# Performance work log

Measured on AMD Instinct MI355X. Metric: run time of the kernel, lower is better.

## Reference

```python
import jax, jax.numpy as jnp
import numpy as np

B, S, D = 512, 64, 2048


def setup_inputs() -> dict:
    key = jax.random.key(0)
    ks = jax.random.split(key, 5)
    return {
        "classical_state": jax.random.normal(ks[0], (B, D), jnp.float32),
        "amplitudes": jax.random.normal(ks[1], (S, D), jnp.float32),
        "phases": jax.random.normal(ks[2], (S, D), jnp.float32),
        "rotation_gates": jax.random.normal(ks[3], (S, 2, 2), jnp.float32),
        "entanglement_matrix": jax.random.normal(ks[4], (S, S), jnp.float32),
    }


def reference(classical_state, amplitudes, phases, rotation_gates, entanglement_matrix):
    # classical_state: [B, D]; amplitudes/phases: [S, D]; rotation_gates: [S, 2, 2]
    b, d = classical_state.shape
    s = amplitudes.shape[0]

    # create_superposition
    norm_amp = amplitudes / jnp.linalg.norm(amplitudes, axis=1, keepdims=True)  # F.normalize p=2 dim=1
    real_amp = norm_amp * (jnp.cos(phases) + jnp.sin(phases))                   # [S, D]

    # _apply_quantum_rotation: per-pair (x[:, 2p:2p+2] @ gate) for each gate i -> vectorized over S and pairs
    xr = classical_state.reshape(b, d // 2, 2)                                  # [B, P, 2]
    rotated = jnp.einsum('bpi,sij->bspj', xr, rotation_gates).reshape(b, s, d)  # [B, S, D]

    states = real_amp[None, :, :] * rotated                                     # weighted superposition [B, S, D]

    # _apply_entanglement: softmax over rows then matmul across superposition dim
    ent_w = jax.nn.softmax(entanglement_matrix, axis=1)                          # [S, S]
    entangled = jnp.einsum('st,btd->bsd', ent_w, states)                         # [B, S, D]

    # collapse_superposition: multinomial over softmax(sum of squares), gather selected state
    logits = jnp.sum(entangled * entangled, axis=2)                              # [B, S]
    probabilities = jax.nn.softmax(logits, axis=1)
    outcome = jax.random.categorical(jax.random.key(42), logits, axis=1)         # [B] ~ multinomial(probabilities)
    collapsed = jnp.take_along_axis(entangled, outcome[:, None, None], axis=1)[:, 0, :]  # [B, D]
    return collapsed
```

## Files before the change

kernel.cpp:

```cpp
#include <hip/hip_runtime.h>
#include <math.h>

#define NB 512
#define NS 64
#define ND 2048
#define NP 1024

__device__ __forceinline__ unsigned rotl32(unsigned x, int d) {
    return (x << d) | (x >> (32 - d));
}

__device__ __forceinline__ void threefry2x32(unsigned k0, unsigned k1,
                                             unsigned& x0, unsigned& x1) {
    const unsigned ks0 = k0, ks1 = k1, ks2 = k0 ^ k1 ^ 0x1BD11BDAu;
    const int r0[4] = {13, 15, 26, 6};
    const int r1[4] = {17, 29, 16, 24};
    x0 += ks0; x1 += ks1;
#pragma unroll
    for (int i = 0; i < 4; ++i) { x0 += x1; x1 = rotl32(x1, r0[i]); x1 ^= x0; }
    x0 += ks1; x1 += ks2 + 1u;
#pragma unroll
    for (int i = 0; i < 4; ++i) { x0 += x1; x1 = rotl32(x1, r1[i]); x1 ^= x0; }
    x0 += ks2; x1 += ks0 + 2u;
#pragma unroll
    for (int i = 0; i < 4; ++i) { x0 += x1; x1 = rotl32(x1, r0[i]); x1 ^= x0; }
    x0 += ks0; x1 += ks1 + 3u;
#pragma unroll
    for (int i = 0; i < 4; ++i) { x0 += x1; x1 = rotl32(x1, r1[i]); x1 ^= x0; }
    x0 += ks1; x1 += ks2 + 4u;
#pragma unroll
    for (int i = 0; i < 4; ++i) { x0 += x1; x1 = rotl32(x1, r0[i]); x1 ^= x0; }
    x0 += ks2; x1 += ks0 + 5u;
}

__global__ void __launch_bounds__(1024)
k_MQ(const float* __restrict__ amp, const float* __restrict__ ph,
     const float* __restrict__ G, const float* __restrict__ E,
     float* __restrict__ M0, float* __restrict__ M1, float* __restrict__ Qt) {
    __shared__ float norm2[NS];
    __shared__ float W_l[NS], in_l[NS];
    __shared__ float Gl[NS * 4];
    __shared__ float4 part4[4][256];
    const int blk = blockIdx.x;
    const int tid = threadIdx.x;
    const int srow = blk >> 2;

    {
        const int r = tid >> 4, sub = tid & 15;
        const float4* a4 = (const float4*)(amp + r * ND);
        float acc = 0.f;
#pragma unroll 8
        for (int i = 0; i < 32; ++i) {
            float4 v = a4[sub + 16 * i];
            acc += v.x * v.x + v.y * v.y + v.z * v.z + v.w * v.w;
        }
        acc += __shfl_down(acc, 8, 16);
        acc += __shfl_down(acc, 4, 16);
        acc += __shfl_down(acc, 2, 16);
        acc += __shfl_down(acc, 1, 16);
        if (sub == 0) norm2[r] = acc;
    }
    if (tid < NS * 4) Gl[tid] = G[tid];
    __syncthreads();
    if (tid < NS) {
        in_l[tid] = 1.0f / sqrtf(norm2[tid]);
        float e = E[srow * NS + tid];
        float m = e;
        for (int off = 32; off; off >>= 1) m = fmaxf(m, __shfl_down(m, off));
        m = __shfl(m, 0);
        float ex = expf(e - m);
        float sum = ex;
        for (int off = 32; off; off >>= 1) sum += __shfl_down(sum, off);
        sum = __shfl(sum, 0);
        W_l[tid] = ex / sum;
    }
    __syncthreads();

    {
        const int pi = tid & 255;
        const int tg = tid >> 8;
        const int p = ((blk & 3) << 8) + pi;
        const int t0 = tg << 4;
        const float2* a2 = (const float2*)amp;
        const float2* p2 = (const float2*)ph;
        float a0 = 0.f, a1 = 0.f, b0 = 0.f, b1 = 0.f;
#pragma unroll 4
        for (int t = t0; t < t0 + 16; ++t) {
            float2 av = a2[t * NP + p];
            float2 pv = p2[t * NP + p];
            float w = W_l[t], in = in_l[t];
            float ra0 = av.x * in * (__cosf(pv.x) + __sinf(pv.x));
            float ra1 = av.y * in * (__cosf(pv.y) + __sinf(pv.y));
            float wr0 = w * ra0, wr1 = w * ra1;
            a0 += wr0 * Gl[4 * t + 0];
            b0 += wr0 * Gl[4 * t + 2];
            a1 += wr1 * Gl[4 * t + 1];
            b1 += wr1 * Gl[4 * t + 3];
        }
        part4[tg][pi] = make_float4(a0, a1, b0, b1);
    }
    __syncthreads();

    if (tid < 256) {
        const int p = ((blk & 3) << 8) + tid;
        float4 s0 = part4[0][tid], s1 = part4[1][tid],
               s2 = part4[2][tid], s3 = part4[3][tid];
        float a0 = s0.x + s1.x + s2.x + s3.x;
        float a1 = s0.y + s1.y + s2.y + s3.y;
        float b0 = s0.z + s1.z + s2.z + s3.z;
        float b1 = s0.w + s1.w + s2.w + s3.w;
        float2 m0v = {a0, a1}, m1v = {b0, b1};
        ((float2*)(M0 + srow * ND))[p] = m0v;
        ((float2*)(M1 + srow * ND))[p] = m1v;
        Qt[(3 * p + 0) * NS + srow] = a0 * a0 + a1 * a1;
        Qt[(3 * p + 1) * NS + srow] = a0 * b0 + a1 * b1;
        Qt[(3 * p + 2) * NS + srow] = b0 * b0 + b1 * b1;
    }
}

__global__ void __launch_bounds__(1024)
k_row(const float* __restrict__ x, const float* __restrict__ Qt,
      const float* __restrict__ M0, const float* __restrict__ M1,
      float* __restrict__ out) {
    __shared__ float2 xs[2 * NP];
    __shared__ float part[16][2][NS];
    __shared__ int o_sh[2];
    const int blk = blockIdx.x;
    const int tid = threadIdx.x;
    const int r0 = 2 * blk;

    ((float4*)xs)[tid] = ((const float4*)(x + r0 * ND))[tid];
    __syncthreads();

    const int w = tid >> 6, s = tid & 63;
    {
        float acc0 = 0.f, acc1 = 0.f;
        const int p0 = w << 6;
#pragma unroll 4
        for (int p = p0; p < p0 + 64; ++p) {
            float q0 = Qt[(3 * p + 0) * NS + s];
            float q1 = Qt[(3 * p + 1) * NS + s];
            float q2 = Qt[(3 * p + 2) * NS + s];
            float2 v0 = xs[p], v1 = xs[NP + p];
            acc0 += v0.x * v0.x * q0 + 2.f * v0.x * v0.y * q1 + v0.y * v0.y * q2;
            acc1 += v1.x * v1.x * q0 + 2.f * v1.x * v1.y * q1 + v1.y * v1.y * q2;
        }
        part[w][0][s] = acc0;
        part[w][1][s] = acc1;
    }
    __syncthreads();

    if (tid < 128) {
        const int w2 = tid >> 6;
        float l = 0.f;
#pragma unroll
        for (int k = 0; k < 16; ++k) l += part[k][w2][s];
        unsigned n = (unsigned)((r0 + w2) * NS + s);
        unsigned t0 = 0u, t1 = n;
        threefry2x32(0u, 42u, t0, t1);
        unsigned bits = t0 ^ t1;
        float u = (float)(bits >> 9) * (1.0f / 8388608.0f);
        u = fmaxf(u, 1.17549435e-38f);
        float g = -logf(-logf(u));
        float best = l + g;
        int bi = s;
        for (int off = 32; off; off >>= 1) {
            float ov = __shfl_down(best, off);
            int oi = __shfl_down(bi, off);
            if (ov > best || (ov == best && oi < bi)) { best = ov; bi = oi; }
        }
        if (s == 0) o_sh[w2] = bi;
    }
    __syncthreads();

#pragma unroll
    for (int r = 0; r < 2; ++r) {
        const int o = o_sh[r];
        const float2* m0p = (const float2*)(M0 + o * ND);
        const float2* m1p = (const float2*)(M1 + o * ND);
        const float2* xr = xs + r * NP;
        float2* op = (float2*)(out + (r0 + r) * ND);
        float2 xv = xr[tid], m0 = m0p[tid], m1 = m1p[tid];
        float2 rr;
        rr.x = xv.x * m0.x + xv.y * m1.x;
        rr.y = xv.x * m0.y + xv.y * m1.y;
        op[tid] = rr;
    }
}

extern "C" void kernel_launch(void* const* d_in, const int* in_sizes, int n_in,
                              void* d_out, int out_size, void* d_ws, size_t ws_size,
                              hipStream_t stream) {
    const float* x   = (const float*)d_in[0];
    const float* amp = (const float*)d_in[1];
    const float* ph  = (const float*)d_in[2];
    const float* G   = (const float*)d_in[3];
    const float* E   = (const float*)d_in[4];
    float* out = (float*)d_out;
    float* ws = (float*)d_ws;

    float* M0 = ws;
    float* M1 = ws + 131072;
    float* Qt = ws + 262144;

    k_MQ <<<256, 1024, 0, stream>>>(amp, ph, G, E, M0, M1, Qt);
    k_row<<<256, 1024, 0, stream>>>(x, Qt, M0, M1, out);
}
```

Measured before the change: 90.58 us.

## Fuse the two kernels into one with a software grid barrier

Merges the precompute kernel (M0/M1/Qt) and the per-row sampling kernel into one persistent launch of 256 blocks. A global atomic counter acts as a grid-wide barrier between the phases, and a second counter resets the barrier state at the end. Shared memory is reused between phases. This removes the second launch and the gap between kernels. It relies on all 256 blocks being resident at once and on the workspace counters starting in a consistent state; otherwise the spin-wait could deadlock.

```diff
diff --git a/kernel.cpp b/kernel.cpp
--- a/kernel.cpp
+++ b/kernel.cpp
@@ -5,6 +5,7 @@
 #define NS 64
 #define ND 2048
 #define NP 1024
+#define NBLK 256
 
 __device__ __forceinline__ unsigned rotl32(unsigned x, int d) {
     return (x << d) | (x >> (32 - d));
@@ -34,15 +35,20 @@
 }
 
 __global__ void __launch_bounds__(1024)
-k_MQ(const float* __restrict__ amp, const float* __restrict__ ph,
-     const float* __restrict__ G, const float* __restrict__ E,
-     float* __restrict__ M0, float* __restrict__ M1, float* __restrict__ Qt) {
+k_fused(const float* __restrict__ x, const float* __restrict__ amp,
+        const float* __restrict__ ph, const float* __restrict__ G,
+        const float* __restrict__ E, float* __restrict__ out,
+        int* __restrict__ bar, float* __restrict__ M0, float* __restrict__ M1,
+        float* __restrict__ Qt) {
+    __shared__ __align__(16) char smem[16384];
     __shared__ float norm2[NS];
     __shared__ float W_l[NS], in_l[NS];
     __shared__ float Gl[NS * 4];
-    __shared__ float4 part4[4][256];
+    __shared__ float partB[16][2][NS];
+    __shared__ int o_sh[2];
     const int blk = blockIdx.x;
     const int tid = threadIdx.x;
+    const int S = *(volatile int*)&bar[0];
     const int srow = blk >> 2;
 
     {
@@ -75,8 +81,8 @@
         W_l[tid] = ex / sum;
     }
     __syncthreads();
-
     {
+        float4* part4 = (float4*)smem;
         const int pi = tid & 255;
         const int tg = tid >> 8;
         const int p = ((blk & 3) << 8) + pi;
@@ -97,14 +103,14 @@
             a1 += wr1 * Gl[4 * t + 1];
             b1 += wr1 * Gl[4 * t + 3];
         }
-        part4[tg][pi] = make_float4(a0, a1, b0, b1);
-    }
-    __syncthreads();
-
+        part4[tg * 256 + pi] = make_float4(a0, a1, b0, b1);
+    }
+    __syncthreads();
     if (tid < 256) {
+        const float4* part4 = (const float4*)smem;
         const int p = ((blk & 3) << 8) + tid;
-        float4 s0 = part4[0][tid], s1 = part4[1][tid],
-               s2 = part4[2][tid], s3 = part4[3][tid];
+        float4 s0 = part4[0 * 256 + tid], s1 = part4[1 * 256 + tid],
+               s2 = part4[2 * 256 + tid], s3 = part4[3 * 256 + tid];
         float a0 = s0.x + s1.x + s2.x + s3.x;
         float a1 = s0.y + s1.y + s2.y + s3.y;
         float b0 = s0.z + s1.z + s2.z + s3.z;
@@ -116,75 +122,87 @@
         Qt[(3 * p + 1) * NS + srow] = a0 * b0 + a1 * b1;
         Qt[(3 * p + 2) * NS + srow] = b0 * b0 + b1 * b1;
     }
-}
-
-__global__ void __launch_bounds__(1024)
-k_row(const float* __restrict__ x, const float* __restrict__ Qt,
-      const float* __restrict__ M0, const float* __restrict__ M1,
-      float* __restrict__ out) {
-    __shared__ float2 xs[2 * NP];
-    __shared__ float part[16][2][NS];
-    __shared__ int o_sh[2];
-    const int blk = blockIdx.x;
-    const int tid = threadIdx.x;
-    const int r0 = 2 * blk;
-
-    ((float4*)xs)[tid] = ((const float4*)(x + r0 * ND))[tid];
-    __syncthreads();
-
-    const int w = tid >> 6, s = tid & 63;
+
+    __syncthreads();
+    if (tid == 0) {
+        __threadfence();
+        atomicAdd(&bar[1], 1);
+        while (__hip_atomic_load(&bar[1], __ATOMIC_RELAXED,
+                                 __HIP_MEMORY_SCOPE_AGENT) != S + NBLK)
+            __builtin_amdgcn_s_sleep(16);
+        __threadfence();
+    }
+    __syncthreads();
+
     {
-        float acc0 = 0.f, acc1 = 0.f;
-        const int p0 = w << 6;
+        float2* xs = (float2*)smem;
+        const int r0 = 2 * blk;
+        ((float4*)xs)[tid] = ((const float4*)(x + r0 * ND))[tid];
+        __syncthreads();
+
+        const int w = tid >> 6, s = tid & 63;
+        {
+            float acc0 = 0.f, acc1 = 0.f;
+            const int p0 = w << 6;
 #pragma unroll 4
-        for (int p = p0; p < p0 + 64; ++p) {
-            float q0 = Qt[(3 * p + 0) * NS + s];
-            float q1 = Qt[(3 * p + 1) * NS + s];
-            float q2 = Qt[(3 * p + 2) * NS + s];
-            float2 v0 = xs[p], v1 = xs[NP + p];
-            acc0 += v0.x * v0.x * q0 + 2.f * v0.x * v0.y * q1 + v0.y * v0.y * q2;
-            acc1 += v1.x * v1.x * q0 + 2.f * v1.x * v1.y * q1 + v1.y * v1.y * q2;
-        }
-        part[w][0][s] = acc0;
-        part[w][1][s] = acc1;
-    }
-    __syncthreads();
-
-    if (tid < 128) {
-        const int w2 = tid >> 6;
-        float l = 0.f;
-#pragma unroll
-        for (int k = 0; k < 16; ++k) l += part[k][w2][s];
-        unsigned n = (unsigned)((r0 + w2) * NS + s);
-        unsigned t0 = 0u, t1 = n;
-        threefry2x32(0u, 42u, t0, t1);
-        unsigned bits = t0 ^ t1;
-        float u = (float)(bits >> 9) * (1.0f / 8388608.0f);
-        u = fmaxf(u, 1.17549435e-38f);
-        float g = -logf(-logf(u));
-        float best = l + g;
-        int bi = s;
-        for (int off = 32; off; off >>= 1) {
-            float ov = __shfl_down(best, off);
-            int oi = __shfl_down(bi, off);
-            if (ov > best || (ov == best && oi < bi)) { best = ov; bi = oi; }
-        }
-        if (s == 0) o_sh[w2] = bi;
-    }
-    __syncthreads();
-
-#pragma unroll
-    for (int r = 0; r < 2; ++r) {
-        const int o = o_sh[r];
-        const float2* m0p = (const float2*)(M0 + o * ND);
-        const float2* m1p = (const float2*)(M1 + o * ND);
-        const float2* xr = xs + r * NP;
-        float2* op = (float2*)(out + (r0 + r) * ND);
-        float2 xv = xr[tid], m0 = m0p[tid], m1 = m1p[tid];
-        float2 rr;
-        rr.x = xv.x * m0.x + xv.y * m1.x;
-        rr.y = xv.x * m0.y + xv.y * m1.y;
-        op[tid] = rr;
+            for (int p = p0; p < p0 + 64; ++p) {
+                float q0 = Qt[(3 * p + 0) * NS + s];
+                float q1 = Qt[(3 * p + 1) * NS + s];
+                float q2 = Qt[(3 * p + 2) * NS + s];
+                float2 v0 = xs[p], v1 = xs[NP + p];
+                acc0 += v0.x * v0.x * q0 + 2.f * v0.x * v0.y * q1 + v0.y * v0.y * q2;
+                acc1 += v1.x * v1.x * q0 + 2.f * v1.x * v1.y * q1 + v1.y * v1.y * q2;
+            }
+            partB[w][0][s] = acc0;
+            partB[w][1][s] = acc1;
+        }
+        __syncthreads();
+
+        if (tid < 128) {
+            const int w2 = tid >> 6;
+            float l = 0.f;
+#pragma unroll
+            for (int k = 0; k < 16; ++k) l += partB[k][w2][s];
+            unsigned n = (unsigned)((r0 + w2) * NS + s);
+            unsigned t0 = 0u, t1 = n;
+            threefry2x32(0u, 42u, t0, t1);
+            unsigned bits = t0 ^ t1;
+            float u = (float)(bits >> 9) * (1.0f / 8388608.0f);
+            u = fmaxf(u, 1.17549435e-38f);
+            float g = -logf(-logf(u));
+            float best = l + g;
+            int bi = s;
+            for (int off = 32; off; off >>= 1) {
+                float ov = __shfl_down(best, off);
+                int oi = __shfl_down(bi, off);
+                if (ov > best || (ov == best && oi < bi)) { best = ov; bi = oi; }
+            }
+            if (s == 0) o_sh[w2] = bi;
+        }
+        __syncthreads();
+
+#pragma unroll
+        for (int r = 0; r < 2; ++r) {
+            const int o = o_sh[r];
+            const float2* m0p = (const float2*)(M0 + o * ND);
+            const float2* m1p = (const float2*)(M1 + o * ND);
+            const float2* xr = xs + r * NP;
+            float2* op = (float2*)(out + (r0 + r) * ND);
+            float2 xv = xr[tid], m0 = m0p[tid], m1 = m1p[tid];
+            float2 rr;
+            rr.x = xv.x * m0.x + xv.y * m1.x;
+            rr.y = xv.x * m0.y + xv.y * m1.y;
+            op[tid] = rr;
+        }
+    }
+
+    if (tid == 0) {
+        __threadfence();
+        int old = atomicAdd(&bar[2], 1);
+        if (old == S + NBLK - 1) {
+            atomicExch(&bar[1], S);
+            atomicExch(&bar[2], S);
+        }
     }
 }
 
@@ -199,10 +217,10 @@
     float* out = (float*)d_out;
     float* ws = (float*)d_ws;
 
-    float* M0 = ws;
-    float* M1 = ws + 131072;
-    float* Qt = ws + 262144;
-
-    k_MQ <<<256, 1024, 0, stream>>>(amp, ph, G, E, M0, M1, Qt);
-    k_row<<<256, 1024, 0, stream>>>(x, Qt, M0, M1, out);
-}
+    int*   bar = (int*)ws;
+    float* M0  = ws + 16;
+    float* M1  = ws + 131088;
+    float* Qt  = ws + 262160;
+
+    k_fused<<<NBLK, 1024, 0, stream>>>(x, amp, ph, G, E, out, bar, M0, M1, Qt);
+}
```

After: 124.6 us. 37.5% more time.
